# Optimization experiments

Hardware: AMD Instinct MI355X
Metric: run time of the kernel (lower is better)

Reference implementation:

```python
import jax, jax.numpy as jnp
import numpy as np

N_NODES = 10000
N_EDGES = 160000
D_IN = 128
D_EMB = 512
D_HID = 256
GAT_SLOPE = 0.2   # PyG GATv2Conv default negative_slope
MLP_SLOPE = 0.1   # relu_alpha


def _glorot(key, shape):
    fan_in, fan_out = shape[0], shape[-1]
    lim = np.sqrt(6.0 / (fan_in + fan_out))
    return jax.random.uniform(key, shape, jnp.float32, -lim, lim)


def setup_inputs() -> dict:
    key = jax.random.key(0)
    ks = jax.random.split(key, 20)
    inp = {
        'x': jax.random.normal(ks[0], (N_NODES, D_IN), jnp.float32),
        'edge_index': jax.random.randint(ks[1], (2, N_EDGES), 0, N_NODES, jnp.int64),
    }
    # GATv2 layers: (Wl, Wr, att, bias) each
    dims = [(D_IN, D_EMB), (D_EMB, D_EMB), (D_EMB, D_EMB)]
    for i, (di, do) in enumerate(dims, start=1):
        inp[f'Wl{i}'] = _glorot(ks[2 + 4 * i], (di, do))
        inp[f'Wr{i}'] = _glorot(ks[3 + 4 * i], (di, do))
        inp[f'att{i}'] = _glorot(ks[4 + 4 * i], (1, do))[0]
        inp[f'b{i}'] = jnp.zeros((do,), jnp.float32)
    # MLP
    inp['A1'] = _glorot(ks[2], (D_EMB, D_HID)); inp['c1'] = jnp.zeros((D_HID,), jnp.float32)
    inp['A2'] = _glorot(ks[3], (D_HID, D_HID)); inp['c2'] = jnp.zeros((D_HID,), jnp.float32)
    inp['A3'] = _glorot(ks[4], (D_HID, 1));     inp['c3'] = jnp.zeros((1,), jnp.float32)
    return inp


def gatv2_conv(x, src, dst, Wl, Wr, att, bias):
    # PyG GATv2Conv, heads=1: xl = source transform, xr = target transform
    xl = x @ Wl                                   # [N, D]
    xr = x @ Wr                                   # [N, D]
    # per-edge attention logit: att . leaky_relu(xl[src] + xr[dst])
    e = jax.nn.leaky_relu(xl[src] + xr[dst], GAT_SLOPE) @ att   # [E]
    # segment softmax over incoming edges of each dst node
    emax = jax.ops.segment_max(e, dst, num_segments=N_NODES)    # [N]
    w = jnp.exp(e - emax[dst])
    denom = jax.ops.segment_sum(w, dst, num_segments=N_NODES)   # [N]
    alpha = w / (denom[dst] + 1e-16)                             # [E]
    out = jax.ops.segment_sum(alpha[:, None] * xl[src], dst, num_segments=N_NODES)
    return out + bias


def reference(x, edge_index, Wl1, Wr1, att1, b1, Wl2, Wr2, att2, b2,
              Wl3, Wr3, att3, b3, A1, c1, A2, c2, A3, c3):
    src, dst = edge_index[0], edge_index[1]
    h = jnp.tanh(gatv2_conv(x, src, dst, Wl1, Wr1, att1, b1))
    h = jnp.tanh(gatv2_conv(h, src, dst, Wl2, Wr2, att2, b2))
    h = jnp.tanh(gatv2_conv(h, src, dst, Wl3, Wr3, att3, b3))
    h = jax.nn.leaky_relu(h @ A1 + c1, MLP_SLOPE)
    h = jax.nn.leaky_relu(h @ A2 + c2, MLP_SLOPE)
    logits = h @ A3 + c3                          # [N, 1]
    return jax.nn.softmax(logits, axis=0)         # softmax over nodes
```

## Files before the change

kernel.cpp:

```cpp
#include <hip/hip_runtime.h>
#include <hip/hip_bf16.h>

#define N_NODES 10000
#define N_EDGES 160000
#define D_IN    128
#define D_EMB   512
#define D_HID   256

typedef unsigned short u16;
typedef __attribute__((ext_vector_type(8))) short short8;
typedef __attribute__((ext_vector_type(4))) float floatx4;

__device__ __forceinline__ float bf2f(u16 u) {
    union { unsigned int i; float f; } v; v.i = ((unsigned int)u) << 16; return v.f;
}
__device__ __forceinline__ u16 f2bf(float f) {
    union { float f; unsigned int i; } v; v.f = f;
    unsigned int x = v.i;
    return (u16)((x + 0x7fffu + ((x >> 16) & 1u)) >> 16);
}
__device__ __forceinline__ float inval(const void* p, int fp32, int idx) {
    return fp32 ? ((const float*)p)[idx] : bf2f(((const u16*)p)[idx]);
}

__device__ __forceinline__ void gld_lds16(const u16* g, u16* l) {
    __builtin_amdgcn_global_load_lds((const __attribute__((address_space(1))) void*)g,
                                     (__attribute__((address_space(3))) void*)l,
                                     16, 0, 0);
}

__device__ __forceinline__ int edge_src(const int* __restrict__ ei, int flg, int e) {
    int v = flg ? ei[2 * e] : ei[e];
    return min(max(v, 0), N_NODES - 1);
}
__device__ __forceinline__ int edge_dst(const int* __restrict__ ei, int flg, int e) {
    int v = flg ? ei[2 * N_EDGES + 2 * e] : ei[N_EDGES + e];
    return min(max(v, 0), N_NODES - 1);
}

__global__ void sentinel_kernel(float* out, int n) {
    int i = blockIdx.x * 256 + threadIdx.x;
    if (i < n) out[i] = 1.0f;
}

__global__ __launch_bounds__(256)
void detect_zero_kernel(const int* __restrict__ ei, const u16* __restrict__ xu,
                        int* flag, int* counts, float* logits) {
    int gid = blockIdx.x * 256 + threadIdx.x;
    for (int i = gid; i < N_NODES; i += gridDim.x * 256) { counts[i] = 0; logits[i] = 0.f; }
    if (blockIdx.x != 0) return;
    __shared__ int s_or[256];
    __shared__ int s_cnt[256];
    int t = threadIdx.x;
    int v = 0;
    for (int k = t; k < 4096; k += 256) v |= ei[1 + 2 * k];
    int c = 0;
    for (int k = t; k < 4096; k += 256) {
        u16 u = xu[k];
        int ex = (u >> 7) & 0xFF;
        bool plaus = (u == 0) || (ex >= 64 && ex <= 191);
        if (!plaus) c++;
    }
    s_or[t] = v; s_cnt[t] = c;
    __syncthreads();
    for (int off = 128; off > 0; off >>= 1) {
        if (t < off) { s_or[t] |= s_or[t + off]; s_cnt[t] += s_cnt[t + off]; }
        __syncthreads();
    }
    if (t == 0) {
        flag[0] = (s_or[0] == 0) ? 1 : 0;
        flag[1] = (s_cnt[0] > 256) ? 1 : 0;
    }
}

struct ConvJobs {
    const void* src[10];
    u16* dh[10];
    u16* dl[10];
    int rows[10], cols[10], trans[10];
    int cum[11];
    int njobs;
};

__global__ __launch_bounds__(256)
void convert_fused_kernel(ConvJobs jobs, const int* __restrict__ flag) {
    int idx = blockIdx.x * 256 + threadIdx.x;
    if (idx >= jobs.cum[jobs.njobs]) return;
    int fp32 = flag[1];
    int jb = 0;
    while (idx >= jobs.cum[jb + 1]) jb++;
    int local = idx - jobs.cum[jb];
    float v = inval(jobs.src[jb], fp32, local);
    u16 hi = f2bf(v);
    int o;
    if (jobs.trans[jb]) {
        int r = local / jobs.cols[jb], c = local % jobs.cols[jb];
        o = c * jobs.rows[jb] + r;
    } else o = local;
    jobs.dh[jb][o] = hi;
    if (jobs.dl[jb]) jobs.dl[jb][o] = f2bf(v - bf2f(hi));
}

__global__ void count_edges_kernel(const int* __restrict__ ei, const int* __restrict__ flag,
                                   int* counts) {
    int e = blockIdx.x * 256 + threadIdx.x;
    if (e < N_EDGES) atomicAdd(&counts[edge_dst(ei, flag[0], e)], 1);
}

__global__ __launch_bounds__(256)
void scan_counts_kernel(int* counts, int* rowptr) {
    __shared__ int part[256];
    int tid = threadIdx.x;
    const int CH = 40;
    int base = tid * CH;
    int loc[CH];
    int s = 0;
    #pragma unroll
    for (int i = 0; i < CH; i++) {
        int idx = base + i;
        int c = (idx < N_NODES) ? counts[idx] : 0;
        loc[i] = s; s += c;
    }
    part[tid] = s;
    __syncthreads();
    for (int off = 1; off < 256; off <<= 1) {
        int v = part[tid];
        int add = (tid >= off) ? part[tid - off] : 0;
        __syncthreads();
        part[tid] = v + add;
        __syncthreads();
    }
    int pre = (tid > 0) ? part[tid - 1] : 0;
    #pragma unroll
    for (int i = 0; i < CH; i++) {
        int idx = base + i;
        if (idx < N_NODES) { int v = pre + loc[i]; rowptr[idx] = v; counts[idx] = v; }
    }
    if (tid == 255) rowptr[N_NODES] = part[255];
}

__global__ void fill_esrcp_kernel(const int* __restrict__ ei, const int* __restrict__ flag,
                                  int* counts, int* esrcp) {
    int e = blockIdx.x * 256 + threadIdx.x;
    if (e < N_EDGES) {
        int flg = flag[0];
        int pos = atomicAdd(&counts[edge_dst(ei, flg, e)], 1);
        if (pos >= 0 && pos < N_EDGES) esrcp[pos] = edge_src(ei, flg, e);
    }
}

__global__ __launch_bounds__(256)
void gemm_dual_kernel(const u16* __restrict__ Ah, const u16* __restrict__ Al,
                      const u16* __restrict__ B0h, const u16* __restrict__ B1h,
                      u16* __restrict__ C0, float* __restrict__ C1,
                      int M, int N, int K)
{
    __shared__ u16 sAh[128 * 32];
    __shared__ u16 sAl[128 * 32];
    __shared__ u16 sBh[128 * 32];
    int nb = N >> 7;
    int half = (int)blockIdx.x >= nb;
    int bx = half ? (blockIdx.x - nb) : blockIdx.x;
    const u16* BTh = half ? B1h : B0h;

    int tid = threadIdx.x;
    int lane = tid & 63, wv = tid >> 6;
    int l15 = lane & 15, l4 = lane >> 4;
    int wr = (wv >> 1) * 64, wc = (wv & 1) * 64;
    int m0 = blockIdx.y * 128, n0 = bx * 128;

    int i0 = tid, i1 = tid + 256;
    int r0 = i0 >> 2, b0 = i0 & 3, sb0 = b0 ^ ((r0 >> 1) & 3);
    int r1 = i1 >> 2, b1 = i1 & 3, sb1 = b1 ^ ((r1 >> 1) & 3);
    int gr0 = min(m0 + r0, M - 1), gr1 = min(m0 + r1, M - 1);
    const u16* a0p = Ah + (size_t)gr0 * K + sb0 * 8;
    const u16* a1p = Ah + (size_t)gr1 * K + sb1 * 8;
    const u16* l0p = Al + (size_t)gr0 * K + sb0 * 8;
    const u16* l1p = Al + (size_t)gr1 * K + sb1 * 8;
    const u16* bb0p = BTh + (size_t)(n0 + r0) * K + sb0 * 8;
    const u16* bb1p = BTh + (size_t)(n0 + r1) * K + sb1 * 8;
    u16* lA0 = &sAh[(size_t)(wv * 64) * 8];
    u16* lA1 = &sAh[(size_t)(256 + wv * 64) * 8];
    u16* lL0 = &sAl[(size_t)(wv * 64) * 8];
    u16* lL1 = &sAl[(size_t)(256 + wv * 64) * 8];
    u16* lB0 = &sBh[(size_t)(wv * 64) * 8];
    u16* lB1 = &sBh[(size_t)(256 + wv * 64) * 8];

    floatx4 acc[4][4];
    #pragma unroll
    for (int i = 0; i < 4; i++)
        #pragma unroll
        for (int j = 0; j < 4; j++) acc[i][j] = (floatx4){0.f, 0.f, 0.f, 0.f};

    int aoff[4], boff[4];
    #pragma unroll
    for (int i = 0; i < 4; i++) {
        int arow = wr + i * 16 + l15;
        aoff[i] = arow * 32 + ((l4 ^ ((arow >> 1) & 3)) << 3);
        int bcol = wc + i * 16 + l15;
        boff[i] = bcol * 32 + ((l4 ^ ((bcol >> 1) & 3)) << 3);
    }

    for (int kk = 0; kk < K; kk += 32) {
        __syncthreads();
        gld_lds16(a0p + kk, lA0);
        gld_lds16(a1p + kk, lA1);
        gld_lds16(l0p + kk, lL0);
        gld_lds16(l1p + kk, lL1);
        gld_lds16(bb0p + kk, lB0);
        gld_lds16(bb1p + kk, lB1);
        __syncthreads();

        short8 ah[4], al[4];
        #pragma unroll
        for (int i = 0; i < 4; i++) {
            ah[i] = *(const short8*)(&sAh[aoff[i]]);
            al[i] = *(const short8*)(&sAl[aoff[i]]);
        }
        #pragma unroll
        for (int j = 0; j < 4; j++) {
            short8 bh = *(const short8*)(&sBh[boff[j]]);
            #pragma unroll
            for (int i = 0; i < 4; i++) {
                acc[i][j] = __builtin_amdgcn_mfma_f32_16x16x32_bf16(ah[i], bh, acc[i][j], 0, 0, 0);
                acc[i][j] = __builtin_amdgcn_mfma_f32_16x16x32_bf16(al[i], bh, acc[i][j], 0, 0, 0);
            }
        }
    }

    #pragma unroll
    for (int j = 0; j < 4; j++) {
        int col = n0 + wc + j * 16 + l15;
        #pragma unroll
        for (int i = 0; i < 4; i++) {
            #pragma unroll
            for (int r = 0; r < 4; r++) {
                int row = m0 + wr + i * 16 + l4 * 4 + r;
                if (row < M) {
                    if (half) C1[(size_t)row * N + col] = acc[i][j][r];
                    else      C0[(size_t)row * N + col] = f2bf(acc[i][j][r]);
                }
            }
        }
    }
}

template<int FUSE>
__global__ __launch_bounds__(256)
void gemm_mlp64_kernel(const u16* __restrict__ Ah, const u16* __restrict__ Al,
                       const u16* __restrict__ BTh,
                       u16* __restrict__ Ch, u16* __restrict__ Cl,
                       const void* __restrict__ biasraw,
                       const void* __restrict__ A3raw, float* __restrict__ logits,
                       const int* __restrict__ flag,
                       int M, int N, int K)
{
    __shared__ u16 sAh[64 * 32];
    __shared__ u16 sAl[64 * 32];
    __shared__ u16 sBh[64 * 32];
    int tid = threadIdx.x;
    int lane = tid & 63, wv = tid >> 6;
    int l15 = lane & 15, l4 = lane >> 4;
    int m0 = blockIdx.y * 64, n0 = blockIdx.x * 64;

    int r = (tid >> 2), blk = tid & 3, sb = blk ^ ((r >> 1) & 3);
    int gr = min(m0 + r, M - 1);
    const u16* ap = Ah + (size_t)gr * K + sb * 8;
    const u16* lp = Al + (size_t)gr * K + sb * 8;
    const u16* bp = BTh + (size_t)(n0 + r) * K + sb * 8;
    u16* lA = &sAh[(size_t)(wv * 64) * 8];
    u16* lL = &sAl[(size_t)(wv * 64) * 8];
    u16* lB = &sBh[(size_t)(wv * 64) * 8];

    floatx4 acc[4];
    #pragma unroll
    for (int j = 0; j < 4; j++) acc[j] = (floatx4){0.f, 0.f, 0.f, 0.f};

    int arow = wv * 16 + l15;
    int aoff = arow * 32 + ((l4 ^ ((arow >> 1) & 3)) << 3);
    int boff[4];
    #pragma unroll
    for (int j = 0; j < 4; j++) {
        int bcol = j * 16 + l15;
        boff[j] = bcol * 32 + ((l4 ^ ((bcol >> 1) & 3)) << 3);
    }

    for (int kk = 0; kk < K; kk += 32) {
        __syncthreads();
        gld_lds16(ap + kk, lA);
        gld_lds16(lp + kk, lL);
        gld_lds16(bp + kk, lB);
        __syncthreads();

        short8 ah = *(const short8*)(&sAh[aoff]);
        short8 al = *(const short8*)(&sAl[aoff]);
        #pragma unroll
        for (int j = 0; j < 4; j++) {
            short8 bh = *(const short8*)(&sBh[boff[j]]);
            acc[j] = __builtin_amdgcn_mfma_f32_16x16x32_bf16(ah, bh, acc[j], 0, 0, 0);
            acc[j] = __builtin_amdgcn_mfma_f32_16x16x32_bf16(al, bh, acc[j], 0, 0, 0);
        }
    }

    const int fp32 = flag[1];
    float lsum[4] = {0.f, 0.f, 0.f, 0.f};
    #pragma unroll
    for (int j = 0; j < 4; j++) {
        int col = n0 + j * 16 + l15;
        float bv = inval(biasraw, fp32, col);
        float a3 = FUSE ? inval(A3raw, fp32, col) : 0.f;
        #pragma unroll
        for (int rr = 0; rr < 4; rr++) {
            int row = m0 + wv * 16 + l4 * 4 + rr;
            if (row < M) {
                float v = acc[j][rr] + bv;
                v = v > 0.f ? v : 0.1f * v;
                if (FUSE) {
                    lsum[rr] += v * a3;
                } else {
                    u16 hi = f2bf(v);
                    Ch[(size_t)row * N + col] = hi;
                    Cl[(size_t)row * N + col] = f2bf(v - bf2f(hi));
                }
            }
        }
    }
    if (FUSE) {
        #pragma unroll
        for (int rr = 0; rr < 4; rr++) {
            float s = lsum[rr];
            s += __shfl_xor(s, 1);
            s += __shfl_xor(s, 2);
            s += __shfl_xor(s, 4);
            s += __shfl_xor(s, 8);
            int row = m0 + wv * 16 + l4 * 4 + rr;
            if (l15 == 0 && row < M) atomicAdd(&logits[row], s);
        }
    }
}

__device__ __forceinline__ void online_update(float e, const float v[8],
                                              float& m_run, float& s_run, float acc[8])
{
    if (e > m_run) {
        float sc = __expf(m_run - e);
        s_run = s_run * sc + 1.f;
        #pragma unroll
        for (int k = 0; k < 8; k++) acc[k] = acc[k] * sc + v[k];
        m_run = e;
    } else {
        float w = __expf(e - m_run);
        s_run += w;
        #pragma unroll
        for (int k = 0; k < 8; k++) acc[k] += w * v[k];
    }
}

__global__ __launch_bounds__(256)
void gat_wave_kernel(const int* __restrict__ rowptr, const int* __restrict__ esrcp,
                     const u16* __restrict__ xlb, const float* __restrict__ xr,
                     const void* __restrict__ att, const void* __restrict__ bias,
                     const int* __restrict__ flag,
                     u16* __restrict__ hh, u16* __restrict__ hl)
{
    int lane = threadIdx.x & 63, wv = threadIdx.x >> 6;
    int n = blockIdx.x * 4 + wv;
    if (n >= N_NODES) return;
    int fp32 = flag[1];
    int d0 = lane * 8;

    const float* xrr = xr + (size_t)n * D_EMB;
    float4 r0 = *(const float4*)(xrr + d0);
    float4 r1 = *(const float4*)(xrr + d0 + 4);
    float xrv[8] = {r0.x, r0.y, r0.z, r0.w, r1.x, r1.y, r1.z, r1.w};
    float attv[8];
    #pragma unroll
    for (int k = 0; k < 8; k++) attv[k] = inval(att, fp32, d0 + k);

    int beg = rowptr[n], end = rowptr[n + 1];
    int deg = end - beg;
    int ngf = deg >> 2;

    float m_run = -3.4e38f, s_run = 0.f;
    float acc[8] = {0.f, 0.f, 0.f, 0.f, 0.f, 0.f, 0.f, 0.f};

    const u16* xbase = xlb + d0;
    int l3 = lane & 3;

    if (ngf > 0) {
        int i0 = esrcp[min(beg + l3, N_EDGES - 1)];
        uint4 cu0, cu1, cu2, cu3;
        {
            int s0 = __shfl(i0, 0), s1 = __shfl(i0, 1), s2 = __shfl(i0, 2), s3 = __shfl(i0, 3);
            cu0 = *(const uint4*)(xbase + (size_t)s0 * D_EMB);
            cu1 = *(const uint4*)(xbase + (size_t)s1 * D_EMB);
            cu2 = *(const uint4*)(xbase + (size_t)s2 * D_EMB);
            cu3 = *(const uint4*)(xbase + (size_t)s3 * D_EMB);
        }
        int nidx = esrcp[min(beg + 4 + l3, N_EDGES - 1)];

        for (int g = 0; g < ngf; g++) {
            uint4 nu0, nu1, nu2, nu3;
            int nidx2 = 0;
            bool have_next = (g + 1 < ngf);
            if (have_next) {
                int t0 = __shfl(nidx, 0), t1 = __shfl(nidx, 1),
                    t2 = __shfl(nidx, 2), t3 = __shfl(nidx, 3);
                nu0 = *(const uint4*)(xbase + (size_t)t0 * D_EMB);
                nu1 = *(const uint4*)(xbase + (size_t)t1 * D_EMB);
                nu2 = *(const uint4*)(xbase + (size_t)t2 * D_EMB);
                nu3 = *(const uint4*)(xbase + (size_t)t3 * D_EMB);
                if (g + 2 < ngf)
                    nidx2 = esrcp[min(beg + 4 * (g + 2) + l3, N_EDGES - 1)];
            }

            union { uint4 q; u16 us[8]; } u0, u1, u2, u3;
            u0.q = cu0; u1.q = cu1; u2.q = cu2; u3.q = cu3;
            float v0[8], v1[8], v2[8], v3[8];
            #pragma unroll
            for (int k = 0; k < 8; k++) {
                v0[k] = bf2f(u0.us[k]); v1[k] = bf2f(u1.us[k]);
                v2[k] = bf2f(u2.us[k]); v3[k] = bf2f(u3.us[k]);
            }
            float e0 = 0.f, e1 = 0.f, e2 = 0.f, e3 = 0.f;
            #pragma unroll
            for (int k = 0; k < 8; k++) {
                float t0 = v0[k] + xrv[k]; t0 = fmaxf(t0, 0.2f * t0); e0 += attv[k] * t0;
                float t1 = v1[k] + xrv[k]; t1 = fmaxf(t1, 0.2f * t1); e1 += attv[k] * t1;
                float t2 = v2[k] + xrv[k]; t2 = fmaxf(t2, 0.2f * t2); e2 += attv[k] * t2;
                float t3 = v3[k] + xrv[k]; t3 = fmaxf(t3, 0.2f * t3); e3 += attv[k] * t3;
            }
            #pragma unroll
            for (int o = 32; o > 0; o >>= 1) {
                e0 += __shfl_xor(e0, o);
                e1 += __shfl_xor(e1, o);
                e2 += __shfl_xor(e2, o);
                e3 += __shfl_xor(e3, o);
            }
            float m4 = fmaxf(fmaxf(e0, e1), fmaxf(e2, e3));
            float m_new = fmaxf(m_run, m4);
            float sc = __expf(m_run - m_new);
            float w0 = __expf(e0 - m_new), w1 = __expf(e1 - m_new);
            float w2 = __expf(e2 - m_new), w3 = __expf(e3 - m_new);
            s_run = s_run * sc + (w0 + w1) + (w2 + w3);
            #pragma unroll
            for (int k = 0; k < 8; k++)
                acc[k] = acc[k] * sc + w0 * v0[k] + w1 * v1[k] + w2 * v2[k] + w3 * v3[k];
            m_run = m_new;

            if (have_next) {
                cu0 = nu0; cu1 = nu1; cu2 = nu2; cu3 = nu3;
                nidx = nidx2;
            }
        }
    }

    for (int j = beg + (ngf << 2); j < end; j++) {
        int sv = esrcp[j];
        union { uint4 q; u16 us[8]; } u0;
        u0.q = *(const uint4*)(xlb + (size_t)sv * D_EMB + d0);
        float v0[8];
        #pragma unroll
        for (int k = 0; k < 8; k++) v0[k] = bf2f(u0.us[k]);
        float e0 = 0.f;
        #pragma unroll
        for (int k = 0; k < 8; k++) {
            float t = v0[k] + xrv[k]; t = fmaxf(t, 0.2f * t); e0 += attv[k] * t;
        }
        #pragma unroll
        for (int o = 32; o > 0; o >>= 1) e0 += __shfl_xor(e0, o);
        online_update(e0, v0, m_run, s_run, acc);
    }

    float inv = 1.f / (s_run + 1e-16f);
    union { uint4 q; u16 us[8]; } ph, pl;
    #pragma unroll
    for (int k = 0; k < 8; k++) {
        float h = tanhf(acc[k] * inv + inval(bias, fp32, d0 + k));
        u16 hi = f2bf(h);
        ph.us[k] = hi;
        pl.us[k] = f2bf(h - bf2f(hi));
    }
    *(uint4*)(&hh[(size_t)n * D_EMB + d0]) = ph.q;
    *(uint4*)(&hl[(size_t)n * D_EMB + d0]) = pl.q;
}

__global__ __launch_bounds__(256)
void softmax_kernel(const float* __restrict__ logits, float* __restrict__ out)
{
    __shared__ float red[4];
    __shared__ float s_m, s_s;
    int tid = threadIdx.x, lane = tid & 63, wv = tid >> 6;
    float m = -3.4e38f;
    for (int i = tid; i < N_NODES; i += 256) m = fmaxf(m, logits[i]);
    #pragma unroll
    for (int o = 32; o > 0; o >>= 1) m = fmaxf(m, __shfl_down(m, o));
    if (lane == 0) red[wv] = m;
    __syncthreads();
    if (tid == 0) {
        float mm = red[0];
        for (int i = 1; i < 4; i++) mm = fmaxf(mm, red[i]);
        s_m = mm;
    }
    __syncthreads();
    float mm = s_m;
    float s = 0.f;
    for (int i = tid; i < N_NODES; i += 256) s += __expf(logits[i] - mm);
    #pragma unroll
    for (int o = 32; o > 0; o >>= 1) s += __shfl_down(s, o);
    if (lane == 0) red[wv] = s;
    __syncthreads();
    if (tid == 0) {
        float ss = 0.f;
        for (int i = 0; i < 4; i++) ss += red[i];
        s_s = ss;
    }
    __syncthreads();
    float invs = 1.f / s_s;
    for (int i = tid; i < N_NODES; i += 256) out[i] = __expf(logits[i] - mm) * invs;
}

extern "C" void kernel_launch(void* const* d_in, const int* in_sizes, int n_in,
                              void* d_out, int out_size, void* d_ws, size_t ws_size,
                              hipStream_t stream)
{
    const void* x   = d_in[0];
    const int*  ei  = (const int*)d_in[1];
    const void* Wl[3]  = {d_in[2],  d_in[6],  d_in[10]};
    const void* Wr[3]  = {d_in[3],  d_in[7],  d_in[11]};
    const void* att[3] = {d_in[4],  d_in[8],  d_in[12]};
    const void* bia[3] = {d_in[5],  d_in[9],  d_in[13]};
    const void* A1 = d_in[14];
    const void* c1 = d_in[15];
    const void* A2 = d_in[16];
    const void* c2 = d_in[17];
    const void* A3 = d_in[18];

    char* p = (char*)d_ws;
    auto alloc = [&](size_t bytes) {
        char* r = p;
        p += (bytes + 255) & ~(size_t)255;
        return r;
    };
    u16*   xlb    = (u16*)  alloc((size_t)N_NODES * D_EMB * 4);
    float* xr     = (float*)alloc((size_t)N_NODES * D_EMB * 4);
    u16*   hh     = (u16*)  alloc((size_t)N_NODES * D_EMB * 2);
    u16*   hl     = (u16*)  alloc((size_t)N_NODES * D_EMB * 2);
    int*   esrcp  = (int*)  alloc((size_t)N_EDGES * 4);
    int*   rowptr = (int*)  alloc((size_t)(N_NODES + 1) * 4);
    int*   counts = (int*)  alloc((size_t)N_NODES * 4);
    int*   flag   = (int*)  alloc(256);
    float* logits = (float*)alloc((size_t)N_NODES * 4);
    u16* wl1h = (u16*)alloc(D_EMB * D_IN  * 2);
    u16* wr1h = (u16*)alloc(D_EMB * D_IN  * 2);
    u16* wl2h = (u16*)alloc(D_EMB * D_EMB * 2);
    u16* wr2h = (u16*)alloc(D_EMB * D_EMB * 2);
    u16* wl3h = (u16*)alloc(D_EMB * D_EMB * 2);
    u16* wr3h = (u16*)alloc(D_EMB * D_EMB * 2);
    u16* a1h  = (u16*)alloc(D_EMB * D_HID * 2);
    u16* a2h  = (u16*)alloc(D_HID * D_HID * 2);
    u16* xph  = (u16*)alloc((size_t)N_NODES * D_IN * 2);
    u16* xpl  = (u16*)alloc((size_t)N_NODES * D_IN * 2);
    size_t needed = (size_t)(p - (char*)d_ws);

    if (ws_size < needed) {
        sentinel_kernel<<<(out_size + 255) / 256, 256, 0, stream>>>((float*)d_out, out_size);
        return;
    }

    u16* m1h = (u16*)xlb;
    u16* m1l = (u16*)((char*)xlb + 5120000);

    detect_zero_kernel<<<40, 256, 0, stream>>>(ei, (const u16*)x, flag, counts, logits);
    count_edges_kernel<<<(N_EDGES + 255) / 256, 256, 0, stream>>>(ei, flag, counts);
    scan_counts_kernel<<<1, 256, 0, stream>>>(counts, rowptr);
    fill_esrcp_kernel<<<(N_EDGES + 255) / 256, 256, 0, stream>>>(ei, flag, counts, esrcp);

    ConvJobs jobs;
    auto setjob = [&](int i, const void* s, u16* dh, u16* dl, int r, int c, int tr) {
        jobs.src[i] = s; jobs.dh[i] = dh; jobs.dl[i] = dl;
        jobs.rows[i] = r; jobs.cols[i] = c; jobs.trans[i] = tr;
    };
    setjob(0, x,     xph,  xpl,     N_NODES, D_IN, 0);
    setjob(1, Wl[0], wl1h, nullptr, D_IN,  D_EMB, 1);
    setjob(2, Wr[0], wr1h, nullptr, D_IN,  D_EMB, 1);
    setjob(3, Wl[1], wl2h, nullptr, D_EMB, D_EMB, 1);
    setjob(4, Wr[1], wr2h, nullptr, D_EMB, D_EMB, 1);
    setjob(5, Wl[2], wl3h, nullptr, D_EMB, D_EMB, 1);
    setjob(6, Wr[2], wr3h, nullptr, D_EMB, D_EMB, 1);
    setjob(7, A1,    a1h,  nullptr, D_EMB, D_HID, 1);
    setjob(8, A2,    a2h,  nullptr, D_HID, D_HID, 1);
    jobs.njobs = 9;
    jobs.cum[0] = 0;
    for (int i = 0; i < 9; i++) jobs.cum[i + 1] = jobs.cum[i] + jobs.rows[i] * jobs.cols[i];
    int ctotal = jobs.cum[9];
    convert_fused_kernel<<<(ctotal + 255) / 256, 256, 0, stream>>>(jobs, flag);

    dim3 gdual(2 * D_EMB / 128, (N_NODES + 127) / 128);
    dim3 gmlp64(D_HID / 64, (N_NODES + 63) / 64);
    int gatgrid = (N_NODES + 3) / 4;

    gemm_dual_kernel<<<gdual, 256, 0, stream>>>(xph, xpl, wl1h, wr1h, xlb, xr, N_NODES, D_EMB, D_IN);
    gat_wave_kernel<<<gatgrid, 256, 0, stream>>>(rowptr, esrcp, xlb, xr, att[0], bia[0], flag, hh, hl);
    gemm_dual_kernel<<<gdual, 256, 0, stream>>>(hh, hl, wl2h, wr2h, xlb, xr, N_NODES, D_EMB, D_EMB);
    gat_wave_kernel<<<gatgrid, 256, 0, stream>>>(rowptr, esrcp, xlb, xr, att[1], bia[1], flag, hh, hl);
    gemm_dual_kernel<<<gdual, 256, 0, stream>>>(hh, hl, wl3h, wr3h, xlb, xr, N_NODES, D_EMB, D_EMB);
    gat_wave_kernel<<<gatgrid, 256, 0, stream>>>(rowptr, esrcp, xlb, xr, att[2], bia[2], flag, hh, hl);

    gemm_mlp64_kernel<0><<<gmlp64, 256, 0, stream>>>(hh, hl, a1h, m1h, m1l, c1, nullptr, nullptr, flag, N_NODES, D_HID, D_EMB);
    gemm_mlp64_kernel<1><<<gmlp64, 256, 0, stream>>>(m1h, m1l, a2h, nullptr, nullptr, c2, A3, logits, flag, N_NODES, D_HID, D_HID);
    softmax_kernel<<<1, 256, 0, stream>>>(logits, (float*)d_out);
}
```

Measured before the change: 423.5 us.

## Sort nodes by degree for GAT aggregation and mask tail edges in 4-groups

Adds a degree histogram, scan and scatter that build a node order sorted by descending in-degree. The GAT aggregation kernel walks nodes in that order, so waves in the same block have similar work and heavy nodes are scheduled first. It also drops the scalar per-edge tail loop: a partial last group of four edges is processed in the vector loop with invalid logits masked to a very negative value. The cost is three extra small kernel launches and less locality in node order when reading xr and writing outputs.

Result: slower. 475.5 us (+12.3%).

```diff
diff --git a/kernel.cpp b/kernel.cpp
--- a/kernel.cpp
+++ b/kernel.cpp
@@ -6,6 +6,7 @@
 #define D_IN    128
 #define D_EMB   512
 #define D_HID   256
+#define DMAX    512
 
 typedef unsigned short u16;
 typedef __attribute__((ext_vector_type(8))) short short8;
@@ -45,9 +46,10 @@
 
 __global__ __launch_bounds__(256)
 void detect_zero_kernel(const int* __restrict__ ei, const u16* __restrict__ xu,
-                        int* flag, int* counts, float* logits) {
+                        int* flag, int* counts, float* logits, int* dhist) {
     int gid = blockIdx.x * 256 + threadIdx.x;
     for (int i = gid; i < N_NODES; i += gridDim.x * 256) { counts[i] = 0; logits[i] = 0.f; }
+    for (int i = gid; i < DMAX; i += gridDim.x * 256) dhist[i] = 0;
     if (blockIdx.x != 0) return;
     __shared__ int s_or[256];
     __shared__ int s_cnt[256];
@@ -146,6 +148,48 @@
         int flg = flag[0];
         int pos = atomicAdd(&counts[edge_dst(ei, flg, e)], 1);
         if (pos >= 0 && pos < N_EDGES) esrcp[pos] = edge_src(ei, flg, e);
+    }
+}
+
+__global__ __launch_bounds__(256)
+void degree_hist_kernel(const int* __restrict__ rowptr, int* __restrict__ dhist) {
+    int n = blockIdx.x * 256 + threadIdx.x;
+    if (n < N_NODES) {
+        int d = min(rowptr[n + 1] - rowptr[n], DMAX - 1);
+        atomicAdd(&dhist[d], 1);
+    }
+}
+
+__global__ __launch_bounds__(256)
+void degree_scan_kernel(const int* __restrict__ dhist, int* __restrict__ doff) {
+    __shared__ int part[256];
+    int tid = threadIdx.x;
+    int d0 = (DMAX - 1) - 2 * tid;
+    int d1 = d0 - 1;
+    int c0 = dhist[d0];
+    int c1 = dhist[d1];
+    part[tid] = c0 + c1;
+    __syncthreads();
+    for (int off = 1; off < 256; off <<= 1) {
+        int v = part[tid];
+        int add = (tid >= off) ? part[tid - off] : 0;
+        __syncthreads();
+        part[tid] = v + add;
+        __syncthreads();
+    }
+    int pre = (tid > 0) ? part[tid - 1] : 0;
+    doff[d0] = pre;
+    doff[d1] = pre + c0;
+}
+
+__global__ __launch_bounds__(256)
+void degree_scatter_kernel(const int* __restrict__ rowptr, int* __restrict__ doff,
+                           int* __restrict__ order) {
+    int n = blockIdx.x * 256 + threadIdx.x;
+    if (n < N_NODES) {
+        int d = min(rowptr[n + 1] - rowptr[n], DMAX - 1);
+        int pos = atomicAdd(&doff[d], 1);
+        if (pos >= 0 && pos < N_NODES) order[pos] = n;
     }
 }
 
@@ -339,35 +383,28 @@
     }
 }
 
-__device__ __forceinline__ void online_update(float e, const float v[8],
-                                              float& m_run, float& s_run, float acc[8])
-{
-    if (e > m_run) {
-        float sc = __expf(m_run - e);
-        s_run = s_run * sc + 1.f;
-        #pragma unroll
-        for (int k = 0; k < 8; k++) acc[k] = acc[k] * sc + v[k];
-        m_run = e;
-    } else {
-        float w = __expf(e - m_run);
-        s_run += w;
-        #pragma unroll
-        for (int k = 0; k < 8; k++) acc[k] += w * v[k];
-    }
-}
-
 __global__ __launch_bounds__(256)
 void gat_wave_kernel(const int* __restrict__ rowptr, const int* __restrict__ esrcp,
+                     const int* __restrict__ order,
                      const u16* __restrict__ xlb, const float* __restrict__ xr,
                      const void* __restrict__ att, const void* __restrict__ bias,
                      const int* __restrict__ flag,
                      u16* __restrict__ hh, u16* __restrict__ hl)
 {
     int lane = threadIdx.x & 63, wv = threadIdx.x >> 6;
-    int n = blockIdx.x * 4 + wv;
-    if (n >= N_NODES) return;
+    int slot = blockIdx.x * 4 + wv;
+    if (slot >= N_NODES) return;
+    int n = order[slot];
+    n = min(max(n, 0), N_NODES - 1);
     int fp32 = flag[1];
     int d0 = lane * 8;
+    int l3 = lane & 3;
+
+    int beg = rowptr[n], end = rowptr[n + 1];
+    int deg = end - beg;
+    int ng = (deg + 3) >> 2;
+
+    const u16* xbase = xlb + d0;
 
     const float* xrr = xr + (size_t)n * D_EMB;
     float4 r0 = *(const float4*)(xrr + d0);
@@ -377,18 +414,15 @@
     #pragma unroll
     for (int k = 0; k < 8; k++) attv[k] = inval(att, fp32, d0 + k);
 
-    int beg = rowptr[n], end = rowptr[n + 1];
-    int deg = end - beg;
-    int ngf = deg >> 2;
-
     float m_run = -3.4e38f, s_run = 0.f;
     float acc[8] = {0.f, 0.f, 0.f, 0.f, 0.f, 0.f, 0.f, 0.f};
 
-    const u16* xbase = xlb + d0;
-    int l3 = lane & 3;
-
-    if (ngf > 0) {
-        int i0 = esrcp[min(beg + l3, N_EDGES - 1)];
+    auto ldidx = [&](int g) -> int {
+        return esrcp[min(beg + 4 * g + l3, N_EDGES - 1)];
+    };
+
+    if (ng > 0) {
+        int i0 = ldidx(0);
         uint4 cu0, cu1, cu2, cu3;
         {
             int s0 = __shfl(i0, 0), s1 = __shfl(i0, 1), s2 = __shfl(i0, 2), s3 = __shfl(i0, 3);
@@ -397,12 +431,12 @@
             cu2 = *(const uint4*)(xbase + (size_t)s2 * D_EMB);
             cu3 = *(const uint4*)(xbase + (size_t)s3 * D_EMB);
         }
-        int nidx = esrcp[min(beg + 4 + l3, N_EDGES - 1)];
-
-        for (int g = 0; g < ngf; g++) {
+        int nidx = (ng > 1) ? ldidx(1) : 0;
+
+        for (int g = 0; g < ng; g++) {
             uint4 nu0, nu1, nu2, nu3;
             int nidx2 = 0;
-            bool have_next = (g + 1 < ngf);
+            bool have_next = (g + 1 < ng);
             if (have_next) {
                 int t0 = __shfl(nidx, 0), t1 = __shfl(nidx, 1),
                     t2 = __shfl(nidx, 2), t3 = __shfl(nidx, 3);
@@ -410,8 +444,7 @@
                 nu1 = *(const uint4*)(xbase + (size_t)t1 * D_EMB);
                 nu2 = *(const uint4*)(xbase + (size_t)t2 * D_EMB);
                 nu3 = *(const uint4*)(xbase + (size_t)t3 * D_EMB);
-                if (g + 2 < ngf)
-                    nidx2 = esrcp[min(beg + 4 * (g + 2) + l3, N_EDGES - 1)];
+                if (g + 2 < ng) nidx2 = ldidx(g + 2);
             }
 
             union { uint4 q; u16 us[8]; } u0, u1, u2, u3;
@@ -437,6 +470,10 @@
                 e2 += __shfl_xor(e2, o);
                 e3 += __shfl_xor(e3, o);
             }
+            int base = beg + 4 * g;
+            if (base + 1 >= end) e1 = -3.4e38f;
+            if (base + 2 >= end) e2 = -3.4e38f;
+            if (base + 3 >= end) e3 = -3.4e38f;
             float m4 = fmaxf(fmaxf(e0, e1), fmaxf(e2, e3));
             float m_new = fmaxf(m_run, m4);
             float sc = __expf(m_run - m_new);
@@ -453,23 +490,6 @@
                 nidx = nidx2;
             }
         }
-    }
-
-    for (int j = beg + (ngf << 2); j < end; j++) {
-        int sv = esrcp[j];
-        union { uint4 q; u16 us[8]; } u0;
-        u0.q = *(const uint4*)(xlb + (size_t)sv * D_EMB + d0);
-        float v0[8];
-        #pragma unroll
-        for (int k = 0; k < 8; k++) v0[k] = bf2f(u0.us[k]);
-        float e0 = 0.f;
-        #pragma unroll
-        for (int k = 0; k < 8; k++) {
-            float t = v0[k] + xrv[k]; t = fmaxf(t, 0.2f * t); e0 += attv[k] * t;
-        }
-        #pragma unroll
-        for (int o = 32; o > 0; o >>= 1) e0 += __shfl_xor(e0, o);
-        online_update(e0, v0, m_run, s_run, acc);
     }
 
     float inv = 1.f / (s_run + 1e-16f);
@@ -551,6 +571,9 @@
     int*   counts = (int*)  alloc((size_t)N_NODES * 4);
     int*   flag   = (int*)  alloc(256);
     float* logits = (float*)alloc((size_t)N_NODES * 4);
+    int*   dhist  = (int*)  alloc(DMAX * 4);
+    int*   doff   = (int*)  alloc(DMAX * 4);
+    int*   order  = (int*)  alloc((size_t)N_NODES * 4);
     u16* wl1h = (u16*)alloc(D_EMB * D_IN  * 2);
     u16* wr1h = (u16*)alloc(D_EMB * D_IN  * 2);
     u16* wl2h = (u16*)alloc(D_EMB * D_EMB * 2);
@@ -571,10 +594,14 @@
     u16* m1h = (u16*)xlb;
     u16* m1l = (u16*)((char*)xlb + 5120000);
 
-    detect_zero_kernel<<<40, 256, 0, stream>>>(ei, (const u16*)x, flag, counts, logits);
+    detect_zero_kernel<<<40, 256, 0, stream>>>(ei, (const u16*)x, flag, counts, logits, dhist);
     count_edges_kernel<<<(N_EDGES + 255) / 256, 256, 0, stream>>>(ei, flag, counts);
     scan_counts_kernel<<<1, 256, 0, stream>>>(counts, rowptr);
     fill_esrcp_kernel<<<(N_EDGES + 255) / 256, 256, 0, stream>>>(ei, flag, counts, esrcp);
+
+    degree_hist_kernel<<<(N_NODES + 255) / 256, 256, 0, stream>>>(rowptr, dhist);
+    degree_scan_kernel<<<1, 256, 0, stream>>>(dhist, doff);
+    degree_scatter_kernel<<<(N_NODES + 255) / 256, 256, 0, stream>>>(rowptr, doff, order);
 
     ConvJobs jobs;
     auto setjob = [&](int i, const void* s, u16* dh, u16* dl, int r, int c, int tr) {
@@ -601,11 +628,11 @@
     int gatgrid = (N_NODES + 3) / 4;
 
     gemm_dual_kernel<<<gdual, 256, 0, stream>>>(xph, xpl, wl1h, wr1h, xlb, xr, N_NODES, D_EMB, D_IN);
-    gat_wave_kernel<<<gatgrid, 256, 0, stream>>>(rowptr, esrcp, xlb, xr, att[0], bia[0], flag, hh, hl);
+    gat_wave_kernel<<<gatgrid, 256, 0, stream>>>(rowptr, esrcp, order, xlb, xr, att[0], bia[0], flag, hh, hl);
     gemm_dual_kernel<<<gdual, 256, 0, stream>>>(hh, hl, wl2h, wr2h, xlb, xr, N_NODES, D_EMB, D_EMB);
-    gat_wave_kernel<<<gatgrid, 256, 0, stream>>>(rowptr, esrcp, xlb, xr, att[1], bia[1], flag, hh, hl);
+    gat_wave_kernel<<<gatgrid, 256, 0, stream>>>(rowptr, esrcp, order, xlb, xr, att[1], bia[1], flag, hh, hl);
     gemm_dual_kernel<<<gdual, 256, 0, stream>>>(hh, hl, wl3h, wr3h, xlb, xr, N_NODES, D_EMB, D_EMB);
-    gat_wave_kernel<<<gatgrid, 256, 0, stream>>>(rowptr, esrcp, xlb, xr, att[2], bia[2], flag, hh, hl);
+    gat_wave_kernel<<<gatgrid, 256, 0, stream>>>(rowptr, esrcp, order, xlb, xr, att[2], bia[2], flag, hh, hl);
 
     gemm_mlp64_kernel<0><<<gmlp64, 256, 0, stream>>>(hh, hl, a1h, m1h, m1l, c1, nullptr, nullptr, flag, N_NODES, D_HID, D_EMB);
     gemm_mlp64_kernel<1><<<gmlp64, 256, 0, stream>>>(m1h, m1l, a2h, nullptr, nullptr, c2, A3, logits, flag, N_NODES, D_HID, D_HID);
```
